# Kernel tuning notes

Hardware: AMD Instinct MI355X
Metric: run time of the kernel (lower is better)

The kernel has to match this reference:

```python
import jax, jax.numpy as jnp
import numpy as np

B, S, DIM, NH = 2, 2048, 1024, 8
DH = DIM // NH
GATE_SOFT_CAP = 15.0
BACKEND_EPS = 5e-05
NORM_EPS = 1e-06


def setup_inputs() -> dict:
    key = jax.random.key(0)
    kq, kk, kv, kw = jax.random.split(key, 4)
    q = jax.random.normal(kq, (B, S, DIM), dtype=jnp.float32)
    k = jax.random.normal(kk, (B, S, DIM), dtype=jnp.float32)
    v = jax.random.normal(kv, (B, S, DIM), dtype=jnp.float32)
    # ifgate: Linear(3*dim, 2*num_heads). Init weight is zeros in the module;
    # use small random weights so the gate path is non-trivial.
    ifgate_w = 0.02 * jax.random.normal(kw, (2 * NH, 3 * DIM), dtype=jnp.float32)
    # bias per reset_parameters: i_bias = -10, f_bias = linspace(3, 6, NH)
    ifgate_b = jnp.concatenate([
        jnp.full((NH,), -10.0, dtype=jnp.float32),
        jnp.linspace(3.0, 6.0, NH, dtype=jnp.float32),
    ])
    # residual-weight RMSNorm gain: effective gain = 1 + outnorm_w (init zeros)
    outnorm_w = jnp.zeros((DIM,), dtype=jnp.float32)
    return {"q": q, "k": k, "v": v, "ifgate_w": ifgate_w,
            "ifgate_b": ifgate_b, "outnorm_w": outnorm_w}


def _mlstm_parallel(q, k, v, i_pre, f_pre):
    # q,k,v: (B,NH,S,DH); i_pre,f_pre: (B,NH,S). Native stabilized parallel mLSTM.
    log_fg = jax.nn.log_sigmoid(f_pre)                       # (B,NH,S)
    lf_cs = jnp.cumsum(log_fg, axis=-1)                      # (B,NH,S)
    lf = jnp.concatenate([jnp.zeros_like(lf_cs[..., :1]), lf_cs], axis=-1)  # (B,NH,S+1)
    # log_D[t, s] = sum_{j=s+1}^{t} log_fg[j] + i_pre[s]  for s <= t, else -inf
    log_d = lf[..., 1:, None] - lf[..., None, 1:] + i_pre[..., None, :]     # (B,NH,S,S)
    t_idx = jnp.arange(q.shape[2])
    mask = t_idx[:, None] >= t_idx[None, :]
    log_d = jnp.where(mask, log_d, -jnp.inf)
    m = jnp.max(log_d, axis=-1, keepdims=True)               # (B,NH,S,1)
    d_mat = jnp.exp(log_d - m)                               # stabilized decays
    scores = jnp.einsum("bhtd,bhsd->bhts", q, k) * (1.0 / np.sqrt(DH))
    s_mat = scores * d_mat                                   # (B,NH,S,S)
    denom = jnp.maximum(jnp.abs(jnp.sum(s_mat, axis=-1, keepdims=True)),
                        jnp.exp(-m)) + BACKEND_EPS
    return jnp.einsum("bhts,bhsd->bhtd", s_mat, v) / denom   # (B,NH,S,DH)


def reference(q, k, v, ifgate_w, ifgate_b, outnorm_w):
    b, s, dim = q.shape
    # gate preactivations from concatenated q,k,v with tanh soft cap
    gate_in = jnp.concatenate([q, k, v], axis=-1)            # (B,S,3*DIM)
    pre = gate_in @ ifgate_w.T + ifgate_b                    # (B,S,2*NH)
    pre = GATE_SOFT_CAP * jnp.tanh(pre / GATE_SOFT_CAP)
    i_pre = pre[..., :NH].transpose(0, 2, 1)                 # (B,NH,S)
    f_pre = pre[..., NH:].transpose(0, 2, 1)                 # (B,NH,S)
    # split heads
    qh = q.reshape(b, s, NH, DH).transpose(0, 2, 1, 3)
    kh = k.reshape(b, s, NH, DH).transpose(0, 2, 1, 3)
    vh = v.reshape(b, s, NH, DH).transpose(0, 2, 1, 3)
    h = _mlstm_parallel(qh, kh, vh, i_pre, f_pre)            # (B,NH,S,DH)
    # multi-head RMSNorm with residual gain (bias is unused in the module's forward)
    rrms = jax.lax.rsqrt(jnp.mean(h * h, axis=-1, keepdims=True) + NORM_EPS)
    gain = (1.0 + outnorm_w).reshape(1, NH, 1, DH)
    h = h * rrms * gain
    return h.transpose(0, 2, 1, 3).reshape(b, s, dim)
```

## Files before the change

### kernel.cpp

```cpp
#include <hip/hip_runtime.h>
#include <math.h>

#define BB 2
#define SS 2048
#define DIMM 1024
#define NHH 8
#define DHH 128
#define NSLOT 51

constexpr float GATE_CAP = 15.0f;
constexpr float B_EPS = 5e-5f;
constexpr float N_EPS = 1e-6f;
constexpr float LOG2E = 1.4426950408889634f;
constexpr float LN_KIS = -2.4260151319598084f;

typedef _Float16 f16x8 __attribute__((ext_vector_type(8)));
typedef __fp16  h16x2 __attribute__((ext_vector_type(2)));
typedef float f32x4 __attribute__((ext_vector_type(4)));

union U8 { f16x8 v; h16x2 h[4]; unsigned int u[4]; };

__device__ __constant__ unsigned char SLOT2QQ[NSLOT] = {
    15,15,15,15,15,15, 14,14,14,14,14, 13,13,13,13,13, 12,12,12,12,12,
    11,11,11,11, 10,10,10,10, 9,9,9,9, 8,8,8, 7,7,7, 6,6,6,
    5,5, 4,4, 3,3, 2, 1, 0};
__device__ __constant__ unsigned char SLOT2CH[NSLOT] = {
    0,1,2,3,4,5, 0,1,2,3,4, 0,1,2,3,4, 0,1,2,3,4,
    0,1,2,3, 0,1,2,3, 0,1,2,3, 0,1,2, 0,1,2, 0,1,2,
    0,1, 0,1, 0,1, 0, 0, 0};
__device__ __constant__ unsigned char QQ2BASE[16] = {50,49,48,46,44,42,39,36,33,29,25,21,16,11,6,0};
__device__ __constant__ unsigned char QQ2NCH[16]  = {1,1,1,2,2,2,3,3,3,4,4,4,5,5,5,6};

__device__ inline unsigned short f2bf(float x) {
    unsigned u = __builtin_bit_cast(unsigned, x);
    unsigned r = (u + 0x7fff + ((u >> 16) & 1)) >> 16;
    return (unsigned short)r;
}
__device__ inline float bf2f(unsigned short s) {
    unsigned u = ((unsigned)s) << 16;
    return __builtin_bit_cast(float, u);
}

#define GLD_LDS16(gsrc, ldst)                                                   \
    __builtin_amdgcn_global_load_lds(                                           \
        (const __attribute__((address_space(1))) unsigned int*)(gsrc),          \
        (__attribute__((address_space(3))) unsigned int*)(ldst), 16, 0, 0)

__global__ __launch_bounds__(256) void gate_kernel(
    const float* __restrict__ q, const float* __restrict__ k, const float* __restrict__ v,
    const float* __restrict__ gw, const float* __restrict__ gb,
    float* __restrict__ i_pre, float* __restrict__ lfcs,
    unsigned short* __restrict__ k16)
{
    __shared__ __align__(16) float xs[2][8][1024];

    const int tid = threadIdx.x;
    const int lane = tid & 63;
    const int wv = tid >> 6;
    const int bs0 = blockIdx.x * 8;

    const float* srcs[3] = {q, k, v};

    auto stage = [&](int buf, int i) {
        const char* src = (const char*)(srcs[i] + (size_t)bs0 * DIMM);
        #pragma unroll
        for (int j = 0; j < 8; ++j) {
            GLD_LDS16(src + j * 4096 + wv * 1024 + lane * 16,
                      (char*)&xs[buf][j][0] + wv * 1024 + lane * 16);
        }
    };

    float acc[8][4];
    #pragma unroll
    for (int r = 0; r < 8; ++r)
        #pragma unroll
        for (int o = 0; o < 4; ++o) acc[r][o] = 0.f;

    stage(0, 0);

    for (int i = 0; i < 3; ++i) {
        const int cur = i & 1;
        const float* gwi = gw + (wv * 4) * 3 * DIMM + i * DIMM;
        float4 w4[4][4];
        #pragma unroll
        for (int step = 0; step < 4; ++step)
            #pragma unroll
            for (int o = 0; o < 4; ++o)
                w4[step][o] = *(const float4*)&gwi[o * 3 * DIMM + step * 256 + lane * 4];

        if (i < 2) {
            stage(cur ^ 1, i + 1);
            asm volatile("s_waitcnt vmcnt(8)" ::: "memory");
        } else {
            asm volatile("s_waitcnt vmcnt(0)" ::: "memory");
        }
        __builtin_amdgcn_s_barrier();
        __builtin_amdgcn_sched_barrier(0);

        #pragma unroll
        for (int step = 0; step < 4; ++step) {
            #pragma unroll
            for (int r = 0; r < 8; ++r) {
                const float4 xv = *(const float4*)&xs[cur][r][step * 256 + lane * 4];
                #pragma unroll
                for (int o = 0; o < 4; ++o)
                    acc[r][o] += xv.x * w4[step][o].x + xv.y * w4[step][o].y
                               + xv.z * w4[step][o].z + xv.w * w4[step][o].w;
            }
        }
        __builtin_amdgcn_s_barrier();
    }

    #pragma unroll
    for (int it = 0; it < 8; ++it) {
        const int item = it * 256 + tid;
        const int r = item >> 8;
        const int dq = item & 255;
        const int hh = dq >> 5;
        const int dd4 = dq & 31;
        float4 kx = *(const float4*)&xs[1][r][dq * 4];
        h16x2 p0 = __builtin_amdgcn_cvt_pkrtz(kx.x, kx.y);
        h16x2 p1 = __builtin_amdgcn_cvt_pkrtz(kx.z, kx.w);
        uint2 wd;
        wd.x = __builtin_bit_cast(unsigned int, p0);
        wd.y = __builtin_bit_cast(unsigned int, p1);
        const int bs = bs0 + r;
        const int b = bs >> 11, s2 = bs & 2047;
        const size_t bh = (size_t)b * NHH + hh;
        *(uint2*)((char*)k16 + (bh * 2048 + s2) * 256 + ((dd4 * 8) ^ ((s2 & 7) << 4))) = wd;
    }

    #pragma unroll
    for (int r = 0; r < 8; ++r)
        #pragma unroll
        for (int o = 0; o < 4; ++o) {
            acc[r][o] += __shfl_xor(acc[r][o], 16);
            acc[r][o] += __shfl_xor(acc[r][o], 32);
        }

    float* scr = &xs[0][0][0];
    const int l16 = lane & 15;
    if (l16 == lane) {
        #pragma unroll
        for (int r = 0; r < 8; ++r) {
            float4 st = {acc[r][0], acc[r][1], acc[r][2], acc[r][3]};
            *(float4*)&scr[wv * 576 + l16 * 36 + r * 4] = st;
        }
    }
    __syncthreads();

    if (tid < 128) {
        const int row = tid & 7, o = tid >> 3;
        const float* base = &scr[(o >> 2) * 576 + row * 4 + (o & 3)];
        float s = 0.f;
        #pragma unroll
        for (int j = 0; j < 16; ++j) s += base[j * 36];
        float p = s + gb[o];
        p = GATE_CAP * tanhf(p / GATE_CAP);
        const int bs = bs0 + row;
        const int b = bs >> 11, s2 = bs & 2047;
        if (o < NHH) {
            i_pre[((size_t)b * NHH + o) * SS + s2] = p;
        } else {
            const int h = o - NHH;
            const float ls = (p >= 0.f) ? -log1pf(expf(-p)) : p - log1pf(expf(p));
            lfcs[((size_t)b * NHH + h) * SS + s2] = ls;
        }
    }
}

__global__ __launch_bounds__(256) void vscan_kernel(
    const float* __restrict__ v, unsigned short* __restrict__ v16,
    const float* __restrict__ i_pre,
    float* __restrict__ lfcs, float* __restrict__ mstab, float* __restrict__ aa)
{
    const int id = blockIdx.x;
    const int tid = threadIdx.x;
    __shared__ float wt[4], wm[4];

    if (id < 512) {
        const int bh = id & 15;
        const int st = id >> 4;
        const int b = bh >> 3, h = bh & 7;
        const int d2 = (tid & 63) * 2;
        const int kb = (tid >> 6) & 1;
        const int gq = tid >> 7;
        const float* vp = v + ((size_t)b * SS + st * 64 + kb * 32) * DIMM + h * DHH + d2;
        char* base = (char*)v16 + ((size_t)bh * 32 + st) * 16384;
        #pragma unroll
        for (int gg = 0; gg < 2; ++gg) {
            const int g = gq * 2 + gg;
            float2 e[8];
            #pragma unroll
            for (int j = 0; j < 8; ++j) {
                const int s = 16 * (j >> 2) + 4 * g + (j & 3);
                e[j] = *(const float2*)&vp[(size_t)s * DIMM];
            }
            U8 u0, u1;
            u0.h[0] = __builtin_amdgcn_cvt_pkrtz(e[0].x, e[1].x);
            u0.h[1] = __builtin_amdgcn_cvt_pkrtz(e[2].x, e[3].x);
            u0.h[2] = __builtin_amdgcn_cvt_pkrtz(e[4].x, e[5].x);
            u0.h[3] = __builtin_amdgcn_cvt_pkrtz(e[6].x, e[7].x);
            u1.h[0] = __builtin_amdgcn_cvt_pkrtz(e[0].y, e[1].y);
            u1.h[1] = __builtin_amdgcn_cvt_pkrtz(e[2].y, e[3].y);
            u1.h[2] = __builtin_amdgcn_cvt_pkrtz(e[4].y, e[5].y);
            u1.h[3] = __builtin_amdgcn_cvt_pkrtz(e[6].y, e[7].y);
            const int p0 = kb * 64 + g * 16;
            *(f16x8*)(base + d2 * 128       + (p0 ^ ((d2 & 7) << 4)))       = u0.v;
            *(f16x8*)(base + (d2 + 1) * 128 + (p0 ^ (((d2 + 1) & 7) << 4))) = u1.v;
        }
        return;
    }

    const int bh = id - 512;
    const int lane = tid & 63, wv = tid >> 6;
    const size_t base = (size_t)bh * SS + tid * 8;

    float x[8];
    {
        float4 a0 = *(const float4*)&lfcs[base];
        float4 a1 = *(const float4*)&lfcs[base + 4];
        x[0] = a0.x; x[1] = a0.y; x[2] = a0.z; x[3] = a0.w;
        x[4] = a1.x; x[5] = a1.y; x[6] = a1.z; x[7] = a1.w;
    }
    #pragma unroll
    for (int i = 1; i < 8; ++i) x[i] += x[i - 1];

    const float tot = x[7];
    float inc = tot;
    #pragma unroll
    for (int off = 1; off < 64; off <<= 1) {
        float n = __shfl_up(inc, off);
        if (lane >= off) inc += n;
    }
    const float exc = inc - tot;

    if (lane == 63) wt[wv] = inc;
    __syncthreads();
    float wpre = 0.f;
    for (int w = 0; w < 4; ++w) if (w < wv) wpre += wt[w];
    const float off0 = exc + wpre;
    #pragma unroll
    for (int i = 0; i < 8; ++i) x[i] += off0;
    {
        float4 s0 = {x[0], x[1], x[2], x[3]}, s1 = {x[4], x[5], x[6], x[7]};
        *(float4*)&lfcs[base] = s0;
        *(float4*)&lfcs[base + 4] = s1;
    }

    float g[8];
    {
        float4 i0 = *(const float4*)&i_pre[base];
        float4 i1 = *(const float4*)&i_pre[base + 4];
        g[0] = i0.x - x[0]; g[1] = i0.y - x[1]; g[2] = i0.z - x[2]; g[3] = i0.w - x[3];
        g[4] = i1.x - x[4]; g[5] = i1.y - x[5]; g[6] = i1.z - x[6]; g[7] = i1.w - x[7];
        float4 s0 = {g[0] * LOG2E, g[1] * LOG2E, g[2] * LOG2E, g[3] * LOG2E};
        float4 s1 = {g[4] * LOG2E, g[5] * LOG2E, g[6] * LOG2E, g[7] * LOG2E};
        *(float4*)&aa[base] = s0;
        *(float4*)&aa[base + 4] = s1;
    }
    float mg[8];
    mg[0] = g[0];
    #pragma unroll
    for (int i = 1; i < 8; ++i) mg[i] = fmaxf(mg[i - 1], g[i]);

    float minc = mg[7];
    #pragma unroll
    for (int off = 1; off < 64; off <<= 1) {
        float n = __shfl_up(minc, off);
        if (lane >= off) minc = fmaxf(minc, n);
    }
    float mexc = __shfl_up(minc, 1);
    if (lane == 0) mexc = -1e30f;
    if (lane == 63) wm[wv] = minc;
    __syncthreads();
    float wmpre = -1e30f;
    for (int w = 0; w < 4; ++w) if (w < wv) wmpre = fmaxf(wmpre, wm[w]);
    const float pm = fmaxf(mexc, wmpre);
    float4 s0, s1;
    s0.x = x[0] + fmaxf(pm, mg[0]); s0.y = x[1] + fmaxf(pm, mg[1]);
    s0.z = x[2] + fmaxf(pm, mg[2]); s0.w = x[3] + fmaxf(pm, mg[3]);
    s1.x = x[4] + fmaxf(pm, mg[4]); s1.y = x[5] + fmaxf(pm, mg[5]);
    s1.z = x[6] + fmaxf(pm, mg[6]); s1.w = x[7] + fmaxf(pm, mg[7]);
    *(float4*)&mstab[base] = s0;
    *(float4*)&mstab[base + 4] = s1;
}

__global__ __launch_bounds__(256, 2) void mlstm_splitk(
    const float* __restrict__ q,
    const unsigned short* __restrict__ k16, const unsigned short* __restrict__ v16,
    const float* __restrict__ lfcs, const float* __restrict__ aa,
    unsigned short* __restrict__ pnum, float* __restrict__ pden)
{
    __shared__ __align__(16) unsigned short kbuf[2][8192];
    __shared__ __align__(16) unsigned short vbuf[2][8192];

    const int tid = threadIdx.x;
    const int lane = tid & 63;
    const int wv = tid >> 6;
    const int g = lane >> 4;
    const int l16 = lane & 15;

    const int id = blockIdx.x;
    const int bh = id & 15;
    const int slot = id >> 4;
    const int qq = SLOT2QQ[slot];
    const int chunk = SLOT2CH[slot];
    const int b = bh >> 3, h = bh & 7;
    const int tw0 = qq * 128 + 32 * wv;

    const size_t bhS = (size_t)bh * SS;
    const float* qp = q + (size_t)b * SS * DIMM + h * DHH;
    const char* kg = (const char*)k16 + (size_t)bh * 524288;
    const char* vg = (const char*)v16 + (size_t)bh * 524288;

    f16x8 qf[2][4];
    float cdec2[2];
    #pragma unroll
    for (int nt = 0; nt < 2; ++nt) {
        const int t = tw0 + 16 * nt + l16;
        cdec2[nt] = (lfcs[bhS + t] + LN_KIS) * LOG2E;
        const float* qrow = qp + (size_t)t * DIMM;
        #pragma unroll
        for (int kb = 0; kb < 4; ++kb) {
            float4 x0 = *(const float4*)&qrow[kb * 32 + g * 8];
            float4 x1 = *(const float4*)&qrow[kb * 32 + g * 8 + 4];
            U8 uu;
            uu.h[0] = __builtin_amdgcn_cvt_pkrtz(x0.x, x0.y);
            uu.h[1] = __builtin_amdgcn_cvt_pkrtz(x0.z, x0.w);
            uu.h[2] = __builtin_amdgcn_cvt_pkrtz(x1.x, x1.y);
            uu.h[3] = __builtin_amdgcn_cvt_pkrtz(x1.z, x1.w);
            qf[nt][kb] = uu.v;
        }
    }

    f32x4 oacc[2][8];
    #pragma unroll
    for (int nt = 0; nt < 2; ++nt)
        #pragma unroll
        for (int mt = 0; mt < 8; ++mt)
            oacc[nt][mt] = (f32x4){0.f, 0.f, 0.f, 0.f};
    float dpart[2] = {0.f, 0.f};

    const int st0 = chunk * 6;
    const int st1m = 2 * qq + 1;
    const int st1 = (st0 + 5 < st1m) ? (st0 + 5) : st1m;

    auto stage = [&](int bi, int st) {
        const char* ksrc = kg + (size_t)st * 16384;
        const char* vsrc = vg + (size_t)st * 16384;
        #pragma unroll
        for (int j = 0; j < 4; ++j) {
            const int off = (j * 4 + wv) * 1024;
            GLD_LDS16(ksrc + off + lane * 16, (char*)&kbuf[bi][0] + off);
            GLD_LDS16(vsrc + off + lane * 16, (char*)&vbuf[bi][0] + off);
        }
    };

    stage(0, st0);

    for (int st = st0; st <= st1; ++st) {
        const int cur = (st - st0) & 1;
        const float* ap = aa + bhS + st * 64;
        f32x4 av[4];
        av[0] = *(const f32x4*)&ap[g * 4];
        av[1] = *(const f32x4*)&ap[16 + g * 4];
        av[2] = *(const f32x4*)&ap[32 + g * 4];
        av[3] = *(const f32x4*)&ap[48 + g * 4];

        if (st < st1) {
            stage(cur ^ 1, st + 1);
            asm volatile("s_waitcnt vmcnt(8)" ::: "memory");
        } else {
            asm volatile("s_waitcnt vmcnt(0)" ::: "memory");
        }
        __builtin_amdgcn_s_barrier();
        __builtin_amdgcn_sched_barrier(0);

        const int s0 = st * 64;
        const bool diag = (st >= 2 * qq);

        f32x4 stacc[2][4];
        #pragma unroll
        for (int nt = 0; nt < 2; ++nt)
            #pragma unroll
            for (int ct = 0; ct < 4; ++ct)
                stacc[nt][ct] = (f32x4){0.f, 0.f, 0.f, 0.f};

        f16x8 pf[2][2];

        #define QKT_PAIR(CT0)                                                            \
            __builtin_amdgcn_s_setprio(1);                                               \
            _Pragma("unroll")                                                            \
            for (int ct = CT0; ct < CT0 + 2; ++ct) {                                     \
                const int row = ct * 16 + l16;                                           \
                _Pragma("unroll")                                                        \
                for (int kb = 0; kb < 4; ++kb) {                                         \
                    f16x8 kf = *(const f16x8*)((const char*)&kbuf[cur][0] +              \
                                ((row * 256 + kb * 64 + g * 16) ^ ((row & 7) << 4)));    \
                    stacc[0][ct] = __builtin_amdgcn_mfma_f32_16x16x32_f16(kf, qf[0][kb], stacc[0][ct], 0, 0, 0); \
                    stacc[1][ct] = __builtin_amdgcn_mfma_f32_16x16x32_f16(kf, qf[1][kb], stacc[1][ct], 0, 0, 0); \
                }                                                                        \
            }                                                                            \
            __builtin_amdgcn_s_setprio(0);

        #define DECAY_PACK(KB)                                                           \
            _Pragma("unroll")                                                            \
            for (int nt = 0; nt < 2; ++nt) {                                             \
                float dsum = 0.f;                                                        \
                const int t_idx = tw0 + nt * 16 + l16;                                   \
                _Pragma("unroll")                                                        \
                for (int ct = 2 * (KB); ct < 2 * (KB) + 2; ++ct) {                       \
                    _Pragma("unroll")                                                    \
                    for (int i = 0; i < 4; ++i) {                                        \
                        const float e = __builtin_amdgcn_exp2f(cdec2[nt] + av[ct][i]);   \
                        float val = stacc[nt][ct][i] * e;                                \
                        if (diag && (s0 + ct * 16 + g * 4 + i > t_idx)) val = 0.f;       \
                        dsum += val;                                                     \
                        stacc[nt][ct][i] = val;                                          \
                    }                                                                    \
                }                                                                        \
                dpart[nt] += dsum;                                                       \
                U8 uu;                                                                   \
                uu.h[0] = __builtin_amdgcn_cvt_pkrtz(stacc[nt][2*(KB)][0],   stacc[nt][2*(KB)][1]);   \
                uu.h[1] = __builtin_amdgcn_cvt_pkrtz(stacc[nt][2*(KB)][2],   stacc[nt][2*(KB)][3]);   \
                uu.h[2] = __builtin_amdgcn_cvt_pkrtz(stacc[nt][2*(KB)+1][0], stacc[nt][2*(KB)+1][1]); \
                uu.h[3] = __builtin_amdgcn_cvt_pkrtz(stacc[nt][2*(KB)+1][2], stacc[nt][2*(KB)+1][3]); \
                pf[nt][KB] = uu.v;                                                       \
            }

        #define PV_HALF(KB)                                                              \
            __builtin_amdgcn_s_setprio(1);                                               \
            _Pragma("unroll")                                                            \
            for (int mt = 0; mt < 8; ++mt) {                                             \
                const int dI = mt * 16 + l16;                                            \
                f16x8 vf = *(const f16x8*)((const char*)&vbuf[cur][0] +                  \
                            dI * 128 + (((KB) * 64 + g * 16) ^ ((dI & 7) << 4)));        \
                oacc[0][mt] = __builtin_amdgcn_mfma_f32_16x16x32_f16(vf, pf[0][KB], oacc[0][mt], 0, 0, 0); \
                oacc[1][mt] = __builtin_amdgcn_mfma_f32_16x16x32_f16(vf, pf[1][KB], oacc[1][mt], 0, 0, 0); \
            }                                                                            \
            __builtin_amdgcn_s_setprio(0);

        QKT_PAIR(0)
        DECAY_PACK(0)
        QKT_PAIR(2)
        PV_HALF(0)
        DECAY_PACK(1)
        PV_HALF(1)

        #undef QKT_PAIR
        #undef DECAY_PACK
        #undef PV_HALF

        __builtin_amdgcn_sched_barrier(0);
        __builtin_amdgcn_s_barrier();
    }

    const size_t cidx = (size_t)bh * NSLOT + slot;
    #pragma unroll
    for (int nt = 0; nt < 2; ++nt) {
        float den = dpart[nt];
        den += __shfl_xor(den, 16);
        den += __shfl_xor(den, 32);
        const int row = wv * 32 + nt * 16 + l16;
        if (g == 0) pden[cidx * 128 + row] = den;
        #pragma unroll
        for (int mt = 0; mt < 8; ++mt) {
            ushort4 pk;
            pk.x = f2bf(oacc[nt][mt][0]);
            pk.y = f2bf(oacc[nt][mt][1]);
            pk.z = f2bf(oacc[nt][mt][2]);
            pk.w = f2bf(oacc[nt][mt][3]);
            *(ushort4*)&pnum[((cidx * 64 + wv * 16 + nt * 8 + mt) << 8) + lane * 4] = pk;
        }
    }
}

__global__ __launch_bounds__(256) void reduce_kernel(
    const unsigned short* __restrict__ pnum, const float* __restrict__ pden,
    const float* __restrict__ mstab, const float* __restrict__ onw,
    float* __restrict__ out)
{
    const int id = blockIdx.x;
    const int bh = id & 15;
    const int qq = id >> 4;
    const int b = bh >> 3, h = bh & 7;
    const int tid = threadIdx.x;
    const int lane = tid & 63;
    const int wv = tid >> 6;
    const int g = lane >> 4;
    const int l16 = lane & 15;

    const int nch = QQ2NCH[qq];
    const size_t cbase = (size_t)bh * NSLOT + QQ2BASE[qq];

    f32x4 acc[2][8];
    #pragma unroll
    for (int nt = 0; nt < 2; ++nt)
        #pragma unroll
        for (int mt = 0; mt < 8; ++mt)
            acc[nt][mt] = (f32x4){0.f, 0.f, 0.f, 0.f};
    float den[2] = {0.f, 0.f};

    for (int c = 0; c < nch; ++c) {
        const size_t fb = (cbase + c) * 64 + wv * 16;
        #pragma unroll
        for (int nt = 0; nt < 2; ++nt) {
            #pragma unroll
            for (int mt = 0; mt < 8; ++mt) {
                ushort4 t4 = *(const ushort4*)&pnum[((fb + nt * 8 + mt) << 8) + lane * 4];
                acc[nt][mt][0] += bf2f(t4.x);
                acc[nt][mt][1] += bf2f(t4.y);
                acc[nt][mt][2] += bf2f(t4.z);
                acc[nt][mt][3] += bf2f(t4.w);
            }
            den[nt] += pden[(cbase + c) * 128 + wv * 32 + nt * 16 + l16];
        }
    }

    #pragma unroll
    for (int nt = 0; nt < 2; ++nt) {
        const int t = qq * 128 + wv * 32 + nt * 16 + l16;
        const float m = mstab[(size_t)bh * SS + t];
        const float em = __expf(-m);
        const float dt = den[nt] * em;
        const float denf = fmaxf(fabsf(dt), em) + B_EPS;
        const float inv = em / denf;
        float ssq = 0.f;
        #pragma unroll
        for (int mt = 0; mt < 8; ++mt) {
            #pragma unroll
            for (int i = 0; i < 4; ++i) {
                acc[nt][mt][i] *= inv;
                ssq += acc[nt][mt][i] * acc[nt][mt][i];
            }
        }
        ssq += __shfl_xor(ssq, 16);
        ssq += __shfl_xor(ssq, 32);
        const float rms = rsqrtf(ssq * (1.0f / DHH) + N_EPS);

        float* orow = out + ((size_t)b * SS + t) * DIMM + h * DHH;
        #pragma unroll
        for (int mt = 0; mt < 8; ++mt) {
            float4 gn = *(const float4*)&onw[h * DHH + mt * 16 + g * 4];
            float4 o4;
            o4.x = acc[nt][mt][0] * rms * (1.f + gn.x);
            o4.y = acc[nt][mt][1] * rms * (1.f + gn.y);
            o4.z = acc[nt][mt][2] * rms * (1.f + gn.z);
            o4.w = acc[nt][mt][3] * rms * (1.f + gn.w);
            *(float4*)&orow[mt * 16 + g * 4] = o4;
        }
    }
}

extern "C" void kernel_launch(void* const* d_in, const int* in_sizes, int n_in,
                              void* d_out, int out_size, void* d_ws, size_t ws_size,
                              hipStream_t stream) {
    const float* q   = (const float*)d_in[0];
    const float* k   = (const float*)d_in[1];
    const float* v   = (const float*)d_in[2];
    const float* gw  = (const float*)d_in[3];
    const float* gb  = (const float*)d_in[4];
    const float* onw = (const float*)d_in[5];
    float* out = (float*)d_out;

    float* ws    = (float*)d_ws;
    float* i_pre = ws;
    float* lfcs  = ws + 32768;
    float* mm    = ws + 65536;
    float* aa    = ws + 98304;
    float* pden  = ws + 131072;
    unsigned short* pnum = (unsigned short*)((char*)d_ws + 1048576);
    unsigned short* k16  = (unsigned short*)((char*)d_ws + 29360128);
    unsigned short* v16  = (unsigned short*)((char*)d_ws + 37748736);

    hipLaunchKernelGGL(gate_kernel, dim3(BB * SS / 8), dim3(256), 0, stream,
                       q, k, v, gw, gb, i_pre, lfcs, k16);
    hipLaunchKernelGGL(vscan_kernel, dim3(528), dim3(256), 0, stream,
                       v, v16, i_pre, lfcs, mm, aa);
    hipLaunchKernelGGL(mlstm_splitk, dim3(16 * NSLOT), dim3(256), 0, stream,
                       q, k16, v16, lfcs, aa, pnum, pden);
    hipLaunchKernelGGL(reduce_kernel, dim3(16 * 16), dim3(256), 0, stream,
                       pnum, pden, mm, onw, out);
}
```

Measured before the change: 76.50 us.

## Use 256-row query tiles with 512-thread blocks and rebalanced split-K slots

The split-K mLSTM kernel now covers 256 query rows per block using 8 waves, so each staged K/V tile in LDS is shared by twice as many query rows. The slot tables are rebuilt to give variable-length key-tile ranges (4-5 tiles) across 32 slots, and the reduce kernel indexes the wider partial layout. A non-diagonal fast path drops the causal mask check. In exchange there are fewer blocks (512 vs 816), which may lower parallelism and worsen tail balance. Launch bounds of 512 threads with 4 blocks per CU also put pressure on the register budget.

New measurement: 256.0 us. +234.7%, slower.

```diff
diff --git a/kernel.cpp b/kernel.cpp
--- a/kernel.cpp
+++ b/kernel.cpp
@@ -6,7 +6,7 @@
 #define DIMM 1024
 #define NHH 8
 #define DHH 128
-#define NSLOT 51
+#define NSLOT 32
 
 constexpr float GATE_CAP = 15.0f;
 constexpr float B_EPS = 5e-5f;
@@ -21,15 +21,13 @@
 union U8 { f16x8 v; h16x2 h[4]; unsigned int u[4]; };
 
 __device__ __constant__ unsigned char SLOT2QQ[NSLOT] = {
-    15,15,15,15,15,15, 14,14,14,14,14, 13,13,13,13,13, 12,12,12,12,12,
-    11,11,11,11, 10,10,10,10, 9,9,9,9, 8,8,8, 7,7,7, 6,6,6,
-    5,5, 4,4, 3,3, 2, 1, 0};
-__device__ __constant__ unsigned char SLOT2CH[NSLOT] = {
-    0,1,2,3,4,5, 0,1,2,3,4, 0,1,2,3,4, 0,1,2,3,4,
-    0,1,2,3, 0,1,2,3, 0,1,2,3, 0,1,2, 0,1,2, 0,1,2,
-    0,1, 0,1, 0,1, 0, 0, 0};
-__device__ __constant__ unsigned char QQ2BASE[16] = {50,49,48,46,44,42,39,36,33,29,25,21,16,11,6,0};
-__device__ __constant__ unsigned char QQ2NCH[16]  = {1,1,1,2,2,2,3,3,3,4,4,4,5,5,5,6};
+    7,7,7,7,7,7,7, 6,6,6,6,6,6, 5,5,5,5,5, 4,4,4,4, 3,3,3,3, 2,2,2, 1,1, 0};
+__device__ __constant__ unsigned char SLOT2ST0[NSLOT] = {
+    0,5,10,15,20,25,30, 0,5,10,15,20,25, 0,5,10,15,20, 0,5,10,15, 0,4,8,12, 0,4,8, 0,4, 0};
+__device__ __constant__ unsigned char SLOT2LEN[NSLOT] = {
+    5,5,5,5,5,5,2, 5,5,5,5,5,3, 5,5,5,5,4, 5,5,5,5, 4,4,4,4, 4,4,4, 4,4, 4};
+__device__ __constant__ unsigned char QQ2BASE[8] = {31,29,26,22,18,13,7,0};
+__device__ __constant__ unsigned char QQ2NCH[8]  = {1,2,3,4,4,5,6,7};
 
 __device__ inline unsigned short f2bf(float x) {
     unsigned u = __builtin_bit_cast(unsigned, x);
@@ -286,7 +284,7 @@
     *(float4*)&mstab[base + 4] = s1;
 }
 
-__global__ __launch_bounds__(256, 2) void mlstm_splitk(
+__global__ __launch_bounds__(512, 4) void mlstm_splitk(
     const float* __restrict__ q,
     const unsigned short* __restrict__ k16, const unsigned short* __restrict__ v16,
     const float* __restrict__ lfcs, const float* __restrict__ aa,
@@ -305,9 +303,10 @@
     const int bh = id & 15;
     const int slot = id >> 4;
     const int qq = SLOT2QQ[slot];
-    const int chunk = SLOT2CH[slot];
+    const int st0 = SLOT2ST0[slot];
+    const int st1 = st0 + SLOT2LEN[slot] - 1;
     const int b = bh >> 3, h = bh & 7;
-    const int tw0 = qq * 128 + 32 * wv;
+    const int tw0 = qq * 256 + 32 * wv;
 
     const size_t bhS = (size_t)bh * SS;
     const float* qp = q + (size_t)b * SS * DIMM + h * DHH;
@@ -342,16 +341,12 @@
             oacc[nt][mt] = (f32x4){0.f, 0.f, 0.f, 0.f};
     float dpart[2] = {0.f, 0.f};
 
-    const int st0 = chunk * 6;
-    const int st1m = 2 * qq + 1;
-    const int st1 = (st0 + 5 < st1m) ? (st0 + 5) : st1m;
-
     auto stage = [&](int bi, int st) {
         const char* ksrc = kg + (size_t)st * 16384;
         const char* vsrc = vg + (size_t)st * 16384;
         #pragma unroll
-        for (int j = 0; j < 4; ++j) {
-            const int off = (j * 4 + wv) * 1024;
+        for (int j = 0; j < 2; ++j) {
+            const int off = (j * 8 + wv) * 1024;
             GLD_LDS16(ksrc + off + lane * 16, (char*)&kbuf[bi][0] + off);
             GLD_LDS16(vsrc + off + lane * 16, (char*)&vbuf[bi][0] + off);
         }
@@ -370,7 +365,7 @@
 
         if (st < st1) {
             stage(cur ^ 1, st + 1);
-            asm volatile("s_waitcnt vmcnt(8)" ::: "memory");
+            asm volatile("s_waitcnt vmcnt(4)" ::: "memory");
         } else {
             asm volatile("s_waitcnt vmcnt(0)" ::: "memory");
         }
@@ -378,7 +373,7 @@
         __builtin_amdgcn_sched_barrier(0);
 
         const int s0 = st * 64;
-        const bool diag = (st >= 2 * qq);
+        const bool diag = (st >= 4 * qq);
 
         f32x4 stacc[2][4];
         #pragma unroll
@@ -404,7 +399,7 @@
             }                                                                            \
             __builtin_amdgcn_s_setprio(0);
 
-        #define DECAY_PACK(KB)                                                           \
+        #define DECAY_PACK(KB, MASKED)                                                   \
             _Pragma("unroll")                                                            \
             for (int nt = 0; nt < 2; ++nt) {                                             \
                 float dsum = 0.f;                                                        \
@@ -415,7 +410,7 @@
                     for (int i = 0; i < 4; ++i) {                                        \
                         const float e = __builtin_amdgcn_exp2f(cdec2[nt] + av[ct][i]);   \
                         float val = stacc[nt][ct][i] * e;                                \
-                        if (diag && (s0 + ct * 16 + g * 4 + i > t_idx)) val = 0.f;       \
+                        if (MASKED && (s0 + ct * 16 + g * 4 + i > t_idx)) val = 0.f;     \
                         dsum += val;                                                     \
                         stacc[nt][ct][i] = val;                                          \
                     }                                                                    \
@@ -441,12 +436,21 @@
             }                                                                            \
             __builtin_amdgcn_s_setprio(0);
 
-        QKT_PAIR(0)
-        DECAY_PACK(0)
-        QKT_PAIR(2)
-        PV_HALF(0)
-        DECAY_PACK(1)
-        PV_HALF(1)
+        if (diag) {
+            QKT_PAIR(0)
+            DECAY_PACK(0, 1)
+            QKT_PAIR(2)
+            PV_HALF(0)
+            DECAY_PACK(1, 1)
+            PV_HALF(1)
+        } else {
+            QKT_PAIR(0)
+            DECAY_PACK(0, 0)
+            QKT_PAIR(2)
+            PV_HALF(0)
+            DECAY_PACK(1, 0)
+            PV_HALF(1)
+        }
 
         #undef QKT_PAIR
         #undef DECAY_PACK
@@ -463,7 +467,7 @@
         den += __shfl_xor(den, 16);
         den += __shfl_xor(den, 32);
         const int row = wv * 32 + nt * 16 + l16;
-        if (g == 0) pden[cidx * 128 + row] = den;
+        if (g == 0) pden[cidx * 256 + row] = den;
         #pragma unroll
         for (int mt = 0; mt < 8; ++mt) {
             ushort4 pk;
@@ -471,7 +475,7 @@
             pk.y = f2bf(oacc[nt][mt][1]);
             pk.z = f2bf(oacc[nt][mt][2]);
             pk.w = f2bf(oacc[nt][mt][3]);
-            *(ushort4*)&pnum[((cidx * 64 + wv * 16 + nt * 8 + mt) << 8) + lane * 4] = pk;
+            *(ushort4*)&pnum[((cidx * 128 + wv * 16 + nt * 8 + mt) << 8) + lane * 4] = pk;
         }
     }
 }
@@ -483,7 +487,9 @@
 {
     const int id = blockIdx.x;
     const int bh = id & 15;
-    const int qq = id >> 4;
+    const int qh = id >> 4;
+    const int qq = qh >> 1;
+    const int half = qh & 1;
     const int b = bh >> 3, h = bh & 7;
     const int tid = threadIdx.x;
     const int lane = tid & 63;
@@ -493,6 +499,7 @@
 
     const int nch = QQ2NCH[qq];
     const size_t cbase = (size_t)bh * NSLOT + QQ2BASE[qq];
+    const int wvS = half * 4 + wv;
 
     f32x4 acc[2][8];
     #pragma unroll
@@ -503,7 +510,7 @@
     float den[2] = {0.f, 0.f};
 
     for (int c = 0; c < nch; ++c) {
-        const size_t fb = (cbase + c) * 64 + wv * 16;
+        const size_t fb = (cbase + c) * 128 + wvS * 16;
         #pragma unroll
         for (int nt = 0; nt < 2; ++nt) {
             #pragma unroll
@@ -514,13 +521,13 @@
                 acc[nt][mt][2] += bf2f(t4.z);
                 acc[nt][mt][3] += bf2f(t4.w);
             }
-            den[nt] += pden[(cbase + c) * 128 + wv * 32 + nt * 16 + l16];
+            den[nt] += pden[(cbase + c) * 256 + wvS * 32 + nt * 16 + l16];
         }
     }
 
     #pragma unroll
     for (int nt = 0; nt < 2; ++nt) {
-        const int t = qq * 128 + wv * 32 + nt * 16 + l16;
+        const int t = qq * 256 + wvS * 32 + nt * 16 + l16;
         const float m = mstab[(size_t)bh * SS + t];
         const float em = __expf(-m);
         const float dt = den[nt] * em;
@@ -571,14 +578,14 @@
     float* aa    = ws + 98304;
     float* pden  = ws + 131072;
     unsigned short* pnum = (unsigned short*)((char*)d_ws + 1048576);
-    unsigned short* k16  = (unsigned short*)((char*)d_ws + 29360128);
-    unsigned short* v16  = (unsigned short*)((char*)d_ws + 37748736);
+    unsigned short* k16  = (unsigned short*)((char*)d_ws + 34603008);
+    unsigned short* v16  = (unsigned short*)((char*)d_ws + 42991616);
 
     hipLaunchKernelGGL(gate_kernel, dim3(BB * SS / 8), dim3(256), 0, stream,
                        q, k, v, gw, gb, i_pre, lfcs, k16);
     hipLaunchKernelGGL(vscan_kernel, dim3(528), dim3(256), 0, stream,
                        v, v16, i_pre, lfcs, mm, aa);
-    hipLaunchKernelGGL(mlstm_splitk, dim3(16 * NSLOT), dim3(256), 0, stream,
+    hipLaunchKernelGGL(mlstm_splitk, dim3(16 * NSLOT), dim3(512), 0, stream,
                        q, k16, v16, lfcs, aa, pnum, pden);
     hipLaunchKernelGGL(reduce_kernel, dim3(16 * 16), dim3(256), 0, stream,
                        pnum, pden, mm, onw, out);
```

## Halve KV tile to 32 keys for four blocks per CU and split diag path

Applied to the files above, without the earlier changes.

The split-k mLSTM kernel now processes 32-key tiles instead of 64, halving the K/V LDS double buffers so launch bounds can request four blocks per CU instead of two. The V fp16 layout written by the scan kernel is changed to match, with 32-key sub-tiles and a smaller XOR swizzle. The decay/mask step is split into separate diagonal and off-diagonal branches so off-diagonal tiles skip the causal comparison. The intent is more latency hiding through occupancy, at the cost of twice as many loop iterations and barriers per chunk and a tighter register budget that could cause spills with the 16 f32x4 output accumulators.

New measurement: 164.6 us. 115% more time.

```diff
diff --git a/kernel.cpp b/kernel.cpp
--- a/kernel.cpp
+++ b/kernel.cpp
@@ -186,7 +186,7 @@
         const int kb = (tid >> 6) & 1;
         const int gq = tid >> 7;
         const float* vp = v + ((size_t)b * SS + st * 64 + kb * 32) * DIMM + h * DHH + d2;
-        char* base = (char*)v16 + ((size_t)bh * 32 + st) * 16384;
+        char* tb = (char*)v16 + (((size_t)bh * 32 + st) * 2 + kb) * 8192;
         #pragma unroll
         for (int gg = 0; gg < 2; ++gg) {
             const int g = gq * 2 + gg;
@@ -205,9 +205,8 @@
             u1.h[1] = __builtin_amdgcn_cvt_pkrtz(e[2].y, e[3].y);
             u1.h[2] = __builtin_amdgcn_cvt_pkrtz(e[4].y, e[5].y);
             u1.h[3] = __builtin_amdgcn_cvt_pkrtz(e[6].y, e[7].y);
-            const int p0 = kb * 64 + g * 16;
-            *(f16x8*)(base + d2 * 128       + (p0 ^ ((d2 & 7) << 4)))       = u0.v;
-            *(f16x8*)(base + (d2 + 1) * 128 + (p0 ^ (((d2 + 1) & 7) << 4))) = u1.v;
+            *(f16x8*)(tb + d2 * 64       + ((g * 16) ^ ((d2 & 3) << 4)))       = u0.v;
+            *(f16x8*)(tb + (d2 + 1) * 64 + ((g * 16) ^ (((d2 + 1) & 3) << 4))) = u1.v;
         }
         return;
     }
@@ -286,14 +285,14 @@
     *(float4*)&mstab[base + 4] = s1;
 }
 
-__global__ __launch_bounds__(256, 2) void mlstm_splitk(
+__global__ __launch_bounds__(256, 4) void mlstm_splitk(
     const float* __restrict__ q,
     const unsigned short* __restrict__ k16, const unsigned short* __restrict__ v16,
     const float* __restrict__ lfcs, const float* __restrict__ aa,
     unsigned short* __restrict__ pnum, float* __restrict__ pden)
 {
-    __shared__ __align__(16) unsigned short kbuf[2][8192];
-    __shared__ __align__(16) unsigned short vbuf[2][8192];
+    __shared__ __align__(16) unsigned short kbuf[2][4096];
+    __shared__ __align__(16) unsigned short vbuf[2][4096];
 
     const int tid = threadIdx.x;
     const int lane = tid & 63;
@@ -342,15 +341,15 @@
             oacc[nt][mt] = (f32x4){0.f, 0.f, 0.f, 0.f};
     float dpart[2] = {0.f, 0.f};
 
-    const int st0 = chunk * 6;
-    const int st1m = 2 * qq + 1;
-    const int st1 = (st0 + 5 < st1m) ? (st0 + 5) : st1m;
+    const int st0 = chunk * 12;
+    const int st1m = 4 * qq + 3;
+    const int st1 = (st0 + 11 < st1m) ? (st0 + 11) : st1m;
 
     auto stage = [&](int bi, int st) {
-        const char* ksrc = kg + (size_t)st * 16384;
-        const char* vsrc = vg + (size_t)st * 16384;
-        #pragma unroll
-        for (int j = 0; j < 4; ++j) {
+        const char* ksrc = kg + (size_t)st * 8192;
+        const char* vsrc = vg + (size_t)st * 8192;
+        #pragma unroll
+        for (int j = 0; j < 2; ++j) {
             const int off = (j * 4 + wv) * 1024;
             GLD_LDS16(ksrc + off + lane * 16, (char*)&kbuf[bi][0] + off);
             GLD_LDS16(vsrc + off + lane * 16, (char*)&vbuf[bi][0] + off);
@@ -361,96 +360,102 @@
 
     for (int st = st0; st <= st1; ++st) {
         const int cur = (st - st0) & 1;
-        const float* ap = aa + bhS + st * 64;
-        f32x4 av[4];
+        const float* ap = aa + bhS + st * 32;
+        f32x4 av[2];
         av[0] = *(const f32x4*)&ap[g * 4];
         av[1] = *(const f32x4*)&ap[16 + g * 4];
-        av[2] = *(const f32x4*)&ap[32 + g * 4];
-        av[3] = *(const f32x4*)&ap[48 + g * 4];
 
         if (st < st1) {
             stage(cur ^ 1, st + 1);
-            asm volatile("s_waitcnt vmcnt(8)" ::: "memory");
+            asm volatile("s_waitcnt vmcnt(4)" ::: "memory");
         } else {
             asm volatile("s_waitcnt vmcnt(0)" ::: "memory");
         }
         __builtin_amdgcn_s_barrier();
         __builtin_amdgcn_sched_barrier(0);
 
-        const int s0 = st * 64;
-        const bool diag = (st >= 2 * qq);
-
-        f32x4 stacc[2][4];
+        const int s0 = st * 32;
+        const bool diag = (st >= 4 * qq);
+
+        f32x4 stacc[2][2];
         #pragma unroll
         for (int nt = 0; nt < 2; ++nt)
             #pragma unroll
-            for (int ct = 0; ct < 4; ++ct)
+            for (int ct = 0; ct < 2; ++ct)
                 stacc[nt][ct] = (f32x4){0.f, 0.f, 0.f, 0.f};
-
-        f16x8 pf[2][2];
-
-        #define QKT_PAIR(CT0)                                                            \
-            __builtin_amdgcn_s_setprio(1);                                               \
-            _Pragma("unroll")                                                            \
-            for (int ct = CT0; ct < CT0 + 2; ++ct) {                                     \
-                const int row = ct * 16 + l16;                                           \
-                _Pragma("unroll")                                                        \
-                for (int kb = 0; kb < 4; ++kb) {                                         \
-                    f16x8 kf = *(const f16x8*)((const char*)&kbuf[cur][0] +              \
-                                ((row * 256 + kb * 64 + g * 16) ^ ((row & 7) << 4)));    \
-                    stacc[0][ct] = __builtin_amdgcn_mfma_f32_16x16x32_f16(kf, qf[0][kb], stacc[0][ct], 0, 0, 0); \
-                    stacc[1][ct] = __builtin_amdgcn_mfma_f32_16x16x32_f16(kf, qf[1][kb], stacc[1][ct], 0, 0, 0); \
-                }                                                                        \
-            }                                                                            \
-            __builtin_amdgcn_s_setprio(0);
-
-        #define DECAY_PACK(KB)                                                           \
-            _Pragma("unroll")                                                            \
-            for (int nt = 0; nt < 2; ++nt) {                                             \
-                float dsum = 0.f;                                                        \
-                const int t_idx = tw0 + nt * 16 + l16;                                   \
-                _Pragma("unroll")                                                        \
-                for (int ct = 2 * (KB); ct < 2 * (KB) + 2; ++ct) {                       \
-                    _Pragma("unroll")                                                    \
-                    for (int i = 0; i < 4; ++i) {                                        \
-                        const float e = __builtin_amdgcn_exp2f(cdec2[nt] + av[ct][i]);   \
-                        float val = stacc[nt][ct][i] * e;                                \
-                        if (diag && (s0 + ct * 16 + g * 4 + i > t_idx)) val = 0.f;       \
-                        dsum += val;                                                     \
-                        stacc[nt][ct][i] = val;                                          \
-                    }                                                                    \
-                }                                                                        \
-                dpart[nt] += dsum;                                                       \
-                U8 uu;                                                                   \
-                uu.h[0] = __builtin_amdgcn_cvt_pkrtz(stacc[nt][2*(KB)][0],   stacc[nt][2*(KB)][1]);   \
-                uu.h[1] = __builtin_amdgcn_cvt_pkrtz(stacc[nt][2*(KB)][2],   stacc[nt][2*(KB)][3]);   \
-                uu.h[2] = __builtin_amdgcn_cvt_pkrtz(stacc[nt][2*(KB)+1][0], stacc[nt][2*(KB)+1][1]); \
-                uu.h[3] = __builtin_amdgcn_cvt_pkrtz(stacc[nt][2*(KB)+1][2], stacc[nt][2*(KB)+1][3]); \
-                pf[nt][KB] = uu.v;                                                       \
-            }
-
-        #define PV_HALF(KB)                                                              \
-            __builtin_amdgcn_s_setprio(1);                                               \
-            _Pragma("unroll")                                                            \
-            for (int mt = 0; mt < 8; ++mt) {                                             \
-                const int dI = mt * 16 + l16;                                            \
-                f16x8 vf = *(const f16x8*)((const char*)&vbuf[cur][0] +                  \
-                            dI * 128 + (((KB) * 64 + g * 16) ^ ((dI & 7) << 4)));        \
-                oacc[0][mt] = __builtin_amdgcn_mfma_f32_16x16x32_f16(vf, pf[0][KB], oacc[0][mt], 0, 0, 0); \
-                oacc[1][mt] = __builtin_amdgcn_mfma_f32_16x16x32_f16(vf, pf[1][KB], oacc[1][mt], 0, 0, 0); \
-            }                                                                            \
-            __builtin_amdgcn_s_setprio(0);
-
-        QKT_PAIR(0)
-        DECAY_PACK(0)
-        QKT_PAIR(2)
-        PV_HALF(0)
-        DECAY_PACK(1)
-        PV_HALF(1)
-
-        #undef QKT_PAIR
-        #undef DECAY_PACK
-        #undef PV_HALF
+        __builtin_amdgcn_s_setprio(1);
+        #pragma unroll
+        for (int ct = 0; ct < 2; ++ct) {
+            const int row = ct * 16 + l16;
+            #pragma unroll
+            for (int kb = 0; kb < 4; ++kb) {
+                f16x8 kf = *(const f16x8*)((const char*)&kbuf[cur][0] +
+                            ((row * 256 + kb * 64 + g * 16) ^ ((row & 7) << 4)));
+                stacc[0][ct] = __builtin_amdgcn_mfma_f32_16x16x32_f16(kf, qf[0][kb], stacc[0][ct], 0, 0, 0);
+                stacc[1][ct] = __builtin_amdgcn_mfma_f32_16x16x32_f16(kf, qf[1][kb], stacc[1][ct], 0, 0, 0);
+            }
+        }
+        __builtin_amdgcn_s_setprio(0);
+
+        f16x8 pf[2];
+        if (diag) {
+            #pragma unroll
+            for (int nt = 0; nt < 2; ++nt) {
+                float dsum = 0.f;
+                const int t_idx = tw0 + nt * 16 + l16;
+                #pragma unroll
+                for (int ct = 0; ct < 2; ++ct) {
+                    #pragma unroll
+                    for (int i = 0; i < 4; ++i) {
+                        const float e = __builtin_amdgcn_exp2f(cdec2[nt] + av[ct][i]);
+                        float val = stacc[nt][ct][i] * e;
+                        if (s0 + ct * 16 + g * 4 + i > t_idx) val = 0.f;
+                        dsum += val;
+                        stacc[nt][ct][i] = val;
+                    }
+                }
+                dpart[nt] += dsum;
+                U8 uu;
+                uu.h[0] = __builtin_amdgcn_cvt_pkrtz(stacc[nt][0][0], stacc[nt][0][1]);
+                uu.h[1] = __builtin_amdgcn_cvt_pkrtz(stacc[nt][0][2], stacc[nt][0][3]);
+                uu.h[2] = __builtin_amdgcn_cvt_pkrtz(stacc[nt][1][0], stacc[nt][1][1]);
+                uu.h[3] = __builtin_amdgcn_cvt_pkrtz(stacc[nt][1][2], stacc[nt][1][3]);
+                pf[nt] = uu.v;
+            }
+        } else {
+            #pragma unroll
+            for (int nt = 0; nt < 2; ++nt) {
+                float dsum = 0.f;
+                #pragma unroll
+                for (int ct = 0; ct < 2; ++ct) {
+                    #pragma unroll
+                    for (int i = 0; i < 4; ++i) {
+                        const float e = __builtin_amdgcn_exp2f(cdec2[nt] + av[ct][i]);
+                        const float val = stacc[nt][ct][i] * e;
+                        dsum += val;
+                        stacc[nt][ct][i] = val;
+                    }
+                }
+                dpart[nt] += dsum;
+                U8 uu;
+                uu.h[0] = __builtin_amdgcn_cvt_pkrtz(stacc[nt][0][0], stacc[nt][0][1]);
+                uu.h[1] = __builtin_amdgcn_cvt_pkrtz(stacc[nt][0][2], stacc[nt][0][3]);
+                uu.h[2] = __builtin_amdgcn_cvt_pkrtz(stacc[nt][1][0], stacc[nt][1][1]);
+                uu.h[3] = __builtin_amdgcn_cvt_pkrtz(stacc[nt][1][2], stacc[nt][1][3]);
+                pf[nt] = uu.v;
+            }
+        }
+
+        __builtin_amdgcn_s_setprio(1);
+        #pragma unroll
+        for (int mt = 0; mt < 8; ++mt) {
+            const int dI = mt * 16 + l16;
+            f16x8 vf = *(const f16x8*)((const char*)&vbuf[cur][0] +
+                        dI * 64 + ((g * 16) ^ ((dI & 3) << 4)));
+            oacc[0][mt] = __builtin_amdgcn_mfma_f32_16x16x32_f16(vf, pf[0], oacc[0][mt], 0, 0, 0);
+            oacc[1][mt] = __builtin_amdgcn_mfma_f32_16x16x32_f16(vf, pf[1], oacc[1][mt], 0, 0, 0);
+        }
+        __builtin_amdgcn_s_setprio(0);
 
         __builtin_amdgcn_sched_barrier(0);
         __builtin_amdgcn_s_barrier();
```
